# Optimization experiments

Hardware: AMD Instinct MI355X
Metric: run time of the kernel (lower is better)

## Reference

```python
import jax, jax.numpy as jnp
import numpy as np

EMBED_DIM = 1024
NUM_HEADS = 16
DEPTH = EMBED_DIM // NUM_HEADS
SCALE_FACTOR = 0.5
SEQ = 2048
BATCH = 2


def setup_inputs() -> dict:
    key = jax.random.key(0)
    ks = jax.random.split(key, 6)
    x = jax.random.normal(ks[0], (SEQ, BATCH, EMBED_DIM), dtype=jnp.float32)
    attn_mask = jnp.zeros((SEQ, SEQ), dtype=jnp.float32)
    key_padding_mask = jnp.zeros((BATCH, SEQ), dtype=bool)
    # Linear params (torch convention: y = x @ W.T + b)
    s_in = 1.0 / np.sqrt(EMBED_DIM)
    qkv_w = jax.random.uniform(ks[1], (3 * EMBED_DIM, EMBED_DIM), jnp.float32, -s_in, s_in)
    qkv_b = jax.random.uniform(ks[2], (3 * EMBED_DIM,), jnp.float32, -s_in, s_in)
    out_w = jax.random.uniform(ks[3], (EMBED_DIM, EMBED_DIM), jnp.float32, -s_in, s_in)
    out_b = jax.random.uniform(ks[4], (EMBED_DIM,), jnp.float32, -s_in, s_in)
    return {"x": x, "attn_mask": attn_mask, "key_padding_mask": key_padding_mask,
            "qkv_w": qkv_w, "qkv_b": qkv_b, "out_w": out_w, "out_b": out_b}


def reference(x, attn_mask, key_padding_mask, qkv_w, qkv_b, out_w, out_b):
    # x: [S, B, E] -> [B, S, E]
    xb = jnp.transpose(x, (1, 0, 2))
    B, S, E = xb.shape
    qkv = xb @ qkv_w.T + qkv_b                       # [B, S, 3E]
    q, k, v = jnp.split(qkv, 3, axis=2)
    def split_heads(t):                              # [B, S, E] -> [B, H, S, d]
        return jnp.transpose(t.reshape(B, S, NUM_HEADS, DEPTH), (0, 2, 1, 3))
    q, k, v = split_heads(q), split_heads(k), split_heads(v)
    scores = jnp.einsum('bhqd,bhkd->bhqk', q, k) / (DEPTH ** SCALE_FACTOR)
    scores = jnp.where(key_padding_mask[:, None, None, :], -jnp.inf, scores)
    scores = scores + attn_mask[None, None, :, :]
    attn = jax.nn.softmax(scores, axis=-1)           # [B, H, S, S] (dropout p=0)
    wa = jnp.einsum('bhqk,bhkd->bhqd', attn, v)      # [B, H, S, d]
    wa = jnp.transpose(wa, (0, 2, 1, 3)).reshape(B, S, E)
    out = wa @ out_w.T + out_b                       # [B, S, E]
    out = jnp.transpose(out, (1, 0, 2))              # [S, B, E]
    attn_mean = jnp.mean(attn, axis=1)               # [B, S, S]
    return out, attn_mean
```

## Files before the change

### kernel.cpp

```cpp
#include <hip/hip_runtime.h>
#include <hip/hip_bf16.h>


#define Sq 2048
#define Bb 2
#define Ee 1024
#define Hh 16
#define Dd 64
#define LOG2E 1.4426950408889634f
#define QSCALE 0.18033688011112042f

typedef __attribute__((ext_vector_type(8))) short bhalf8;
typedef __attribute__((ext_vector_type(4))) float f32x4;

__device__ __forceinline__ void gld16(const __hip_bfloat16* g, __hip_bfloat16* l) {
    __builtin_amdgcn_global_load_lds(
        (const __attribute__((address_space(1))) unsigned int*)g,
        (__attribute__((address_space(3))) unsigned int*)l, 16, 0, 0);
}

__device__ __forceinline__ int pkbf(float a, float b) {
    union { __hip_bfloat16 h[2]; int i; } u;
    u.h[0] = __float2bfloat16(a);
    u.h[1] = __float2bfloat16(b);
    return u.i;
}

__device__ __forceinline__ int tile_off(int s) {
    return ((s >> 2) & 1) * 2048 + (s >> 7) * 512 + (s & 3) * 128 + ((s >> 3) & 15) * 8;
}

__device__ __forceinline__ int swz(int t) {
    return (t & ~63) | ((t & 7) << 3) | ((t >> 3) & 7);
}

__device__ __forceinline__ int kperm(int p) {
    return (p & 3) | (((p >> 5) & 1) << 2) | ((p & 12) << 1) | (((p >> 4) & 1) << 5);
}

__global__ __launch_bounds__(256) void prep_k(
    const float* __restrict__ x, const float* __restrict__ am,
    const unsigned int* __restrict__ kpm32,
    const float* __restrict__ qkv_w, const float* __restrict__ out_w,
    __hip_bfloat16* __restrict__ xb, __hip_bfloat16* __restrict__ qwb,
    __hip_bfloat16* __restrict__ owb, unsigned int* __restrict__ flag)
{
    const long i = (long)blockIdx.x*256 + threadIdx.x;
    if (i < 1048576) {
        float4 v = ((const float4*)am)[i];
        bool nz = (v.x != 0.f) | (v.y != 0.f) | (v.z != 0.f) | (v.w != 0.f);
        if (i < 1024) nz |= (kpm32[i] != 0u);
        if (__ballot(nz)) { if ((threadIdx.x & 63) == 0) atomicOr(flag, 1u); }
    } else if (i < 2097152) {
        const long j = i - 1048576;
        const int m = (int)(j >> 8), e4 = (int)(j & 255);
        const int b = m >> 11, s = m & 2047;
        float4 v = ((const float4*)x)[(size_t)(s*Bb + b)*256 + e4];
        union { __hip_bfloat16 h[4]; uint2 u; } o;
        o.h[0]=__float2bfloat16(v.x); o.h[1]=__float2bfloat16(v.y);
        o.h[2]=__float2bfloat16(v.z); o.h[3]=__float2bfloat16(v.w);
        ((uint2*)xb)[(size_t)m*256 + e4] = o.u;
    } else if (i < 2883584) {
        const long j = i - 2097152;
        float4 v = ((const float4*)qkv_w)[j];
        union { __hip_bfloat16 h[4]; uint2 u; } o;
        o.h[0]=__float2bfloat16(v.x); o.h[1]=__float2bfloat16(v.y);
        o.h[2]=__float2bfloat16(v.z); o.h[3]=__float2bfloat16(v.w);
        ((uint2*)qwb)[j] = o.u;
    } else if (i < 3145728) {
        const long j = i - 2883584;
        float4 v = ((const float4*)out_w)[j];
        union { __hip_bfloat16 h[4]; uint2 u; } o;
        o.h[0]=__float2bfloat16(v.x); o.h[1]=__float2bfloat16(v.y);
        o.h[2]=__float2bfloat16(v.z); o.h[3]=__float2bfloat16(v.w);
        ((uint2*)owb)[j] = o.u;
    }
}

__global__ __launch_bounds__(256) void gemm_qkv(
    const __hip_bfloat16* __restrict__ A, const __hip_bfloat16* __restrict__ Bw,
    const float* __restrict__ bias,
    __hip_bfloat16* __restrict__ Qp, __hip_bfloat16* __restrict__ Kp,
    __hip_bfloat16* __restrict__ Vt)
{
    __shared__ __align__(16) __hip_bfloat16 As[128*32];
    __shared__ __align__(16) __hip_bfloat16 Bs[128*32];
    const int t = threadIdx.x;
    const int l = t & 63, lm = l & 15, quad = l >> 4;
    const int w = t >> 6;
    const int mw = (w & 1)*64, nw = (w >> 1)*64;
    const int m0 = blockIdx.y*128, n0 = blockIdx.x*128;

    const int srow = t >> 2;
    const int scol = (t & 3)*8;
    const __hip_bfloat16* ag = A  + (size_t)(m0 + srow)*1024 + scol;
    const __hip_bfloat16* bg = Bw + (size_t)(n0 + srow)*1024 + scol;
    __hip_bfloat16* al = As + t*8;
    __hip_bfloat16* bl = Bs + t*8;

    f32x4 acc[4][4] = {};
    for (int k0 = 0; k0 < 1024; k0 += 32) {
        __syncthreads();
        gld16(ag + k0, al);
        gld16(ag + (size_t)64*1024 + k0, al + 2048);
        gld16(bg + k0, bl);
        gld16(bg + (size_t)64*1024 + k0, bl + 2048);
        __syncthreads();
        bhalf8 af[4], bf[4];
#pragma unroll
        for (int i = 0; i < 4; i++) {
            af[i] = *(const bhalf8*)&As[(mw + i*16 + lm)*32 + quad*8];
            bf[i] = *(const bhalf8*)&Bs[(nw + i*16 + lm)*32 + quad*8];
        }
#pragma unroll
        for (int mf = 0; mf < 4; mf++)
#pragma unroll
            for (int nf = 0; nf < 4; nf++)
                acc[mf][nf] = __builtin_amdgcn_mfma_f32_16x16x32_bf16(af[mf], bf[nf], acc[mf][nf], 0,0,0);
    }
#pragma unroll
    for (int nf = 0; nf < 4; nf++) {
        const int n = n0 + nw + nf*16 + lm;
        const float bz = bias[n];
        const int which = n >> 10, hh = (n >> 6) & 15, dd = n & 63;
#pragma unroll
        for (int mf = 0; mf < 4; mf++)
#pragma unroll
            for (int r = 0; r < 4; r++) {
                const int m = m0 + mw + mf*16 + quad*4 + r;
                const int b2 = m >> 11, s2 = m & 2047;
                const float vf = acc[mf][nf][r] + bz;
                if (which == 0)
                    Qp[((size_t)(b2*Hh + hh)*Sq + s2)*Dd + dd] = __float2bfloat16(vf * QSCALE);
                else if (which == 1)
                    Kp[((size_t)(b2*Hh + hh)*Sq + s2)*Dd + dd] = __float2bfloat16(vf);
                else
                    Vt[((size_t)(b2*Hh + hh)*Dd + dd)*Sq + s2] = __float2bfloat16(vf);
            }
    }
}

__global__ __launch_bounds__(256) void attn_mfma(
    const __hip_bfloat16* __restrict__ Qp, const __hip_bfloat16* __restrict__ Kp,
    const __hip_bfloat16* __restrict__ Vt,
    const float* __restrict__ am, const unsigned char* __restrict__ kpm,
    const unsigned int* __restrict__ flag,
    __hip_bfloat16* __restrict__ wa, float* __restrict__ rlbuf)
{
    __shared__ __align__(16) __hip_bfloat16 Ks[4096];
    __shared__ __align__(16) __hip_bfloat16 Vs[4096];
    const int t = threadIdx.x;
    const int w = t >> 6, l = t & 63, lm = l & 15, quad = l >> 4;
    const int blk = blockIdx.x;
    const int xcd = blk & 7;
    const int qt  = (blk >> 3) & 15;
    const int grp = blk >> 7;
    const int bh  = grp*8 + xcd;
    const int b   = bh >> 4, h = bh & 15;
    const int q0  = qt*128 + w*16;
    const bool masked = (flag[0] != 0u);

    const __hip_bfloat16* qbase = Qp + (size_t)bh*Sq*Dd;
    const __hip_bfloat16* kbase = Kp + (size_t)bh*Sq*Dd;
    const __hip_bfloat16* vbase = Vt + (size_t)bh*Dd*Sq;

    bhalf8 bq[2][2];
#pragma unroll
    for (int su = 0; su < 2; su++) {
        const int q = q0 + su*64 + lm;
        bq[su][0] = *(const bhalf8*)(qbase + (size_t)q*Dd + quad*8);
        bq[su][1] = *(const bhalf8*)(qbase + (size_t)q*Dd + quad*8 + 32);
    }

    f32x4 o[2][4] = {};
    float lsum[2] = {0.f, 0.f};

    const int g0 = swz(t), g1 = g0 + 256;
    const int off0 = tile_off(g0), off1 = tile_off(g1);
    const int krow0 = kperm(g0 >> 3);
    const int krow1 = kperm(g1 >> 3);
    const int kcol  = (g0 & 7)*8;
    const int vrow0 = g0 >> 3, vrow1 = g1 >> 3;

    uint4 kreg0 = *(const uint4*)(kbase + (size_t)krow0*Dd + kcol);
    uint4 kreg1 = *(const uint4*)(kbase + (size_t)krow1*Dd + kcol);
    uint4 vreg0 = *(const uint4*)(vbase + (size_t)vrow0*Sq + kcol);
    uint4 vreg1 = *(const uint4*)(vbase + (size_t)vrow1*Sq + kcol);

    for (int kt = 0; kt < 32; kt++) {
        __syncthreads();
        *(uint4*)&Ks[off0] = kreg0;
        *(uint4*)&Ks[off1] = kreg1;
        *(uint4*)&Vs[off0] = vreg0;
        *(uint4*)&Vs[off1] = vreg1;
        if (kt < 31) {
            const int kn = (kt + 1)*64;
            kreg0 = *(const uint4*)(kbase + (size_t)(kn + krow0)*Dd + kcol);
            kreg1 = *(const uint4*)(kbase + (size_t)(kn + krow1)*Dd + kcol);
            vreg0 = *(const uint4*)(vbase + (size_t)vrow0*Sq + kn + kcol);
            vreg1 = *(const uint4*)(vbase + (size_t)vrow1*Sq + kn + kcol);
        }
        __syncthreads();

        const int k0 = kt*64;
        f32x4 s[2][4] = {};
#pragma unroll
        for (int f = 0; f < 2; f++) {
            bhalf8 ak[4];
#pragma unroll
            for (int j = 0; j < 4; j++)
                ak[j] = *(const bhalf8*)&Ks[f*2048 + j*512 + l*8];
#pragma unroll
            for (int su = 0; su < 2; su++)
#pragma unroll
                for (int j = 0; j < 4; j++)
                    s[su][j] = __builtin_amdgcn_mfma_f32_16x16x32_bf16(ak[j], bq[su][f], s[su][j], 0,0,0);
        }

        int pk[2][4][2];
#pragma unroll
        for (int su = 0; su < 2; su++) {
            const int q = q0 + su*64 + lm;
#pragma unroll
            for (int j = 0; j < 4; j++) {
                float p[4];
#pragma unroll
                for (int r = 0; r < 4; r++) {
                    float sv = s[su][j][r];
                    if (masked) {
                        const int key = k0 + 32*(j & 1) + 8*quad + 4*(j >> 1) + r;
                        const float km = kpm[b*Sq + key] ? -1e30f : 0.0f;
                        sv += (am[(size_t)q*Sq + key] + km) * LOG2E;
                    }
                    p[r] = exp2f(sv);
                }
                lsum[su] += (p[0]+p[1]) + (p[2]+p[3]);
                pk[su][j][0] = pkbf(p[0], p[1]);
                pk[su][j][1] = pkbf(p[2], p[3]);
            }
        }

#pragma unroll
        for (int ks = 0; ks < 2; ks++) {
            bhalf8 av[4];
#pragma unroll
            for (int nd = 0; nd < 4; nd++)
                av[nd] = *(const bhalf8*)&Vs[ks*2048 + nd*512 + l*8];
#pragma unroll
            for (int su = 0; su < 2; su++) {
                union { int i[4]; bhalf8 v; } bp;
                bp.i[0] = pk[su][ks][0];
                bp.i[1] = pk[su][ks][1];
                bp.i[2] = pk[su][ks + 2][0];
                bp.i[3] = pk[su][ks + 2][1];
#pragma unroll
                for (int nd = 0; nd < 4; nd++)
                    o[su][nd] = __builtin_amdgcn_mfma_f32_16x16x32_bf16(av[nd], bp.v, o[su][nd], 0,0,0);
            }
        }
    }

#pragma unroll
    for (int su = 0; su < 2; su++) {
        const int q = q0 + su*64 + lm;
        float ls = lsum[su];
        ls += __shfl_xor(ls, 16, 64);
        ls += __shfl_xor(ls, 32, 64);
        const float rl = 1.0f / ls;
        if (quad == 0) rlbuf[(size_t)bh*Sq + q] = rl * 0.0625f;
#pragma unroll
        for (int nd = 0; nd < 4; nd++) {
            union { __hip_bfloat16 hx[4]; uint2 u; } ou;
#pragma unroll
            for (int r = 0; r < 4; r++) ou.hx[r] = __float2bfloat16(o[su][nd][r] * rl);
            *(uint2*)(wa + ((size_t)b*Sq + q)*Ee + h*Dd + nd*16 + quad*4) = ou.u;
        }
    }
}

__global__ __launch_bounds__(256) void attn_mean_k(
    const __hip_bfloat16* __restrict__ Qp, const __hip_bfloat16* __restrict__ Kp,
    const float* __restrict__ am, const unsigned char* __restrict__ kpm,
    const unsigned int* __restrict__ flag,
    const float* __restrict__ rlbuf, float* __restrict__ attn_mean)
{
    __shared__ __align__(16) __hip_bfloat16 Ks[2][4096];
    const int t = threadIdx.x;
    const int w = t >> 6, l = t & 63, lm = l & 15, quad = l >> 4;
    const int blk = blockIdx.x;
    const int q0idx = (blk & 7) | (((blk >> 8) & 1) << 3);
    const int kc    = ((blk >> 3) & 31) * 64;
    const int b     = (blk >> 9) & 1;
    const int q0    = q0idx * 128;
    const bool masked = (flag[0] != 0u);

    const int g0 = swz(t), g1 = g0 + 256;
    const int off0 = tile_off(g0), off1 = tile_off(g1);
    const int qa = q0 + w*32;

    float macc[2][4][4] = {};
    uint4 kr0, kr1;

    {
        const __hip_bfloat16* kg = Kp + ((size_t)(b*Hh)*Sq + kc)*Dd;
        uint4 a0 = *(const uint4*)(kg + (size_t)g0*8);
        uint4 a1 = *(const uint4*)(kg + (size_t)g1*8);
        *(uint4*)&Ks[0][off0] = a0;
        *(uint4*)&Ks[0][off1] = a1;
        const __hip_bfloat16* kg1 = kg + (size_t)Sq*Dd;
        kr0 = *(const uint4*)(kg1 + (size_t)g0*8);
        kr1 = *(const uint4*)(kg1 + (size_t)g1*8);
    }

    for (int h = 0; h < Hh; h++) {
        __syncthreads();
        if (h < Hh - 1) {
            *(uint4*)&Ks[(h + 1) & 1][off0] = kr0;
            *(uint4*)&Ks[(h + 1) & 1][off1] = kr1;
            if (h < Hh - 2) {
                const __hip_bfloat16* kn = Kp + ((size_t)(b*Hh + h + 2)*Sq + kc)*Dd;
                kr0 = *(const uint4*)(kn + (size_t)g0*8);
                kr1 = *(const uint4*)(kn + (size_t)g1*8);
            }
        }

        const size_t base = (size_t)(b*Hh + h)*Sq;
        const __hip_bfloat16* Kc = Ks[h & 1];
#pragma unroll
        for (int su = 0; su < 2; su++) {
            const int qrow = qa + su*16;
            const __hip_bfloat16* qg = Qp + (base + qrow + lm)*Dd + quad*8;
            f32x4 s[4] = {};
#pragma unroll
            for (int f = 0; f < 2; f++) {
                bhalf8 aq = *(const bhalf8*)(qg + f*32);
#pragma unroll
                for (int j = 0; j < 4; j++) {
                    bhalf8 bk = *(const bhalf8*)&Kc[f*2048 + j*512 + l*8];
                    s[j] = __builtin_amdgcn_mfma_f32_16x16x32_bf16(aq, bk, s[j], 0,0,0);
                }
            }
            const f32x4 rl4 = *(const f32x4*)(rlbuf + base + qrow + quad*4);
#pragma unroll
            for (int j = 0; j < 4; j++)
#pragma unroll
                for (int r = 0; r < 4; r++) {
                    float sv = s[j][r];
                    if (masked) {
                        const int key = kc + j*16 + lm;
                        const float km = kpm[b*Sq + key] ? -1e30f : 0.0f;
                        sv += (am[(size_t)(qrow + quad*4 + r)*Sq + key] + km) * LOG2E;
                    }
                    macc[su][j][r] += exp2f(sv) * rl4[r];
                }
        }
    }

#pragma unroll
    for (int su = 0; su < 2; su++)
#pragma unroll
        for (int j = 0; j < 4; j++)
#pragma unroll
            for (int r = 0; r < 4; r++)
                attn_mean[((size_t)b*Sq + qa + su*16 + quad*4 + r)*Sq + kc + j*16 + lm] =
                    macc[su][j][r];
}

__global__ __launch_bounds__(256) void gemm_out(
    const __hip_bfloat16* __restrict__ A, const __hip_bfloat16* __restrict__ Bw,
    const float* __restrict__ bias, float* __restrict__ outp)
{
    __shared__ __align__(16) __hip_bfloat16 As[128*32];
    __shared__ __align__(16) __hip_bfloat16 Bs[128*32];
    const int t = threadIdx.x;
    const int l = t & 63, lm = l & 15, quad = l >> 4;
    const int w = t >> 6;
    const int mw = (w & 1)*64, nw = (w >> 1)*64;
    const int m0 = blockIdx.y*128, n0 = blockIdx.x*128;

    const int srow = t >> 2;
    const int scol = (t & 3)*8;
    const __hip_bfloat16* ag = A  + (size_t)(m0 + srow)*1024 + scol;
    const __hip_bfloat16* bg = Bw + (size_t)(n0 + srow)*1024 + scol;
    __hip_bfloat16* al = As + t*8;
    __hip_bfloat16* bl = Bs + t*8;

    f32x4 acc[4][4] = {};
    for (int k0 = 0; k0 < 1024; k0 += 32) {
        __syncthreads();
        gld16(ag + k0, al);
        gld16(ag + (size_t)64*1024 + k0, al + 2048);
        gld16(bg + k0, bl);
        gld16(bg + (size_t)64*1024 + k0, bl + 2048);
        __syncthreads();
        bhalf8 af[4], bf[4];
#pragma unroll
        for (int i = 0; i < 4; i++) {
            af[i] = *(const bhalf8*)&As[(mw + i*16 + lm)*32 + quad*8];
            bf[i] = *(const bhalf8*)&Bs[(nw + i*16 + lm)*32 + quad*8];
        }
#pragma unroll
        for (int mf = 0; mf < 4; mf++)
#pragma unroll
            for (int nf = 0; nf < 4; nf++)
                acc[mf][nf] = __builtin_amdgcn_mfma_f32_16x16x32_bf16(af[mf], bf[nf], acc[mf][nf], 0,0,0);
    }
#pragma unroll
    for (int nf = 0; nf < 4; nf++) {
        const int n = n0 + nw + nf*16 + lm;
        const float bz = bias[n];
#pragma unroll
        for (int mf = 0; mf < 4; mf++)
#pragma unroll
            for (int r = 0; r < 4; r++) {
                const int m = m0 + mw + mf*16 + quad*4 + r;
                const int b2 = m >> 11, s2 = m & 2047;
                outp[((size_t)s2*Bb + b2)*Ee + n] = acc[mf][nf][r] + bz;
            }
    }
}

extern "C" void kernel_launch(void* const* d_in, const int* in_sizes, int n_in,
                              void* d_out, int out_size, void* d_ws, size_t ws_size,
                              hipStream_t stream) {
    const float*         x         = (const float*)d_in[0];
    const float*         attn_mask = (const float*)d_in[1];
    const unsigned char* kpm       = (const unsigned char*)d_in[2];
    const float*         qkv_w     = (const float*)d_in[3];
    const float*         qkv_b     = (const float*)d_in[4];
    const float*         out_w     = (const float*)d_in[5];
    const float*         out_b     = (const float*)d_in[6];

    float* outp      = (float*)d_out;
    float* attn_mean = outp + 4194304;

    __hip_bfloat16* xb  = (__hip_bfloat16*)d_ws;
    __hip_bfloat16* qwb = xb  + 4194304;
    __hip_bfloat16* owb = qwb + 3145728;
    __hip_bfloat16* Qp  = owb + 1048576;
    __hip_bfloat16* Kp  = Qp  + 4194304;
    __hip_bfloat16* Vt  = Kp  + 4194304;
    __hip_bfloat16* wab = Vt  + 4194304;
    float* rlbuf        = (float*)(wab + 4194304);
    unsigned int* flag  = (unsigned int*)(rlbuf + 65536);

    hipMemsetAsync(flag, 0, sizeof(unsigned int), stream);
    prep_k<<<12288, 256, 0, stream>>>(x, attn_mask, (const unsigned int*)kpm,
                                      qkv_w, out_w, xb, qwb, owb, flag);
    gemm_qkv<<<dim3(24, 32), 256, 0, stream>>>(xb, qwb, qkv_b, Qp, Kp, Vt);
    attn_mfma<<<dim3(512), 256, 0, stream>>>(Qp, Kp, Vt, attn_mask, kpm, flag, wab, rlbuf);
    attn_mean_k<<<dim3(1024), 256, 0, stream>>>(Qp, Kp, attn_mask, kpm, flag, rlbuf, attn_mean);
    gemm_out<<<dim3(8, 32), 256, 0, stream>>>(wab, owb, out_b, outp);
}
```

Measured before the change: 314.4 us.

## Load K/V MFMA operands directly from global, drop LDS staging and barriers

The attention kernel stops staging K and V tiles through shared memory with double-buffered registers and two barriers per iteration. Each wave now loads its MFMA operands straight from global memory (relying on L2/L1 reuse across waves) and raises wave priority around the MFMA blocks. Float-to-bf16 packing is switched to the hardware packed-convert instruction everywhere. The trade is more global/L1 traffic and exposed load latency with no explicit prefetch, in exchange for no LDS writes or block-wide syncs.

```diff
diff --git a/kernel.cpp b/kernel.cpp
--- a/kernel.cpp
+++ b/kernel.cpp
@@ -20,10 +20,9 @@
 }
 
 __device__ __forceinline__ int pkbf(float a, float b) {
-    union { __hip_bfloat16 h[2]; int i; } u;
-    u.h[0] = __float2bfloat16(a);
-    u.h[1] = __float2bfloat16(b);
-    return u.i;
+    int r;
+    asm("v_cvt_pk_bf16_f32 %0, %1, %2" : "=v"(r) : "v"(a), "v"(b));
+    return r;
 }
 
 __device__ __forceinline__ int tile_off(int s) {
@@ -32,10 +31,6 @@
 
 __device__ __forceinline__ int swz(int t) {
     return (t & ~63) | ((t & 7) << 3) | ((t >> 3) & 7);
-}
-
-__device__ __forceinline__ int kperm(int p) {
-    return (p & 3) | (((p >> 5) & 1) << 2) | ((p & 12) << 1) | (((p >> 4) & 1) << 5);
 }
 
 __global__ __launch_bounds__(256) void prep_k(
@@ -56,24 +51,24 @@
         const int m = (int)(j >> 8), e4 = (int)(j & 255);
         const int b = m >> 11, s = m & 2047;
         float4 v = ((const float4*)x)[(size_t)(s*Bb + b)*256 + e4];
-        union { __hip_bfloat16 h[4]; uint2 u; } o;
-        o.h[0]=__float2bfloat16(v.x); o.h[1]=__float2bfloat16(v.y);
-        o.h[2]=__float2bfloat16(v.z); o.h[3]=__float2bfloat16(v.w);
-        ((uint2*)xb)[(size_t)m*256 + e4] = o.u;
+        uint2 o;
+        o.x = (unsigned)pkbf(v.x, v.y);
+        o.y = (unsigned)pkbf(v.z, v.w);
+        ((uint2*)xb)[(size_t)m*256 + e4] = o;
     } else if (i < 2883584) {
         const long j = i - 2097152;
         float4 v = ((const float4*)qkv_w)[j];
-        union { __hip_bfloat16 h[4]; uint2 u; } o;
-        o.h[0]=__float2bfloat16(v.x); o.h[1]=__float2bfloat16(v.y);
-        o.h[2]=__float2bfloat16(v.z); o.h[3]=__float2bfloat16(v.w);
-        ((uint2*)qwb)[j] = o.u;
+        uint2 o;
+        o.x = (unsigned)pkbf(v.x, v.y);
+        o.y = (unsigned)pkbf(v.z, v.w);
+        ((uint2*)qwb)[j] = o;
     } else if (i < 3145728) {
         const long j = i - 2883584;
         float4 v = ((const float4*)out_w)[j];
-        union { __hip_bfloat16 h[4]; uint2 u; } o;
-        o.h[0]=__float2bfloat16(v.x); o.h[1]=__float2bfloat16(v.y);
-        o.h[2]=__float2bfloat16(v.z); o.h[3]=__float2bfloat16(v.w);
-        ((uint2*)owb)[j] = o.u;
+        uint2 o;
+        o.x = (unsigned)pkbf(v.x, v.y);
+        o.y = (unsigned)pkbf(v.z, v.w);
+        ((uint2*)owb)[j] = o;
     }
 }
 
@@ -147,8 +142,6 @@
     const unsigned int* __restrict__ flag,
     __hip_bfloat16* __restrict__ wa, float* __restrict__ rlbuf)
 {
-    __shared__ __align__(16) __hip_bfloat16 Ks[4096];
-    __shared__ __align__(16) __hip_bfloat16 Vs[4096];
     const int t = threadIdx.x;
     const int w = t >> 6, l = t & 63, lm = l & 15, quad = l >> 4;
     const int blk = blockIdx.x;
@@ -172,50 +165,40 @@
         bq[su][1] = *(const bhalf8*)(qbase + (size_t)q*Dd + quad*8 + 32);
     }
 
+    int krA[4];
+#pragma unroll
+    for (int j = 0; j < 4; j++)
+        krA[j] = (lm & 3) | ((j >> 1) << 2) | ((lm & 12) << 1) | ((j & 1) << 5);
+    const __hip_bfloat16* pK = kbase + quad*8;
+    const __hip_bfloat16* pV = vbase + (size_t)lm*Sq + quad*8;
+
     f32x4 o[2][4] = {};
     float lsum[2] = {0.f, 0.f};
 
-    const int g0 = swz(t), g1 = g0 + 256;
-    const int off0 = tile_off(g0), off1 = tile_off(g1);
-    const int krow0 = kperm(g0 >> 3);
-    const int krow1 = kperm(g1 >> 3);
-    const int kcol  = (g0 & 7)*8;
-    const int vrow0 = g0 >> 3, vrow1 = g1 >> 3;
-
-    uint4 kreg0 = *(const uint4*)(kbase + (size_t)krow0*Dd + kcol);
-    uint4 kreg1 = *(const uint4*)(kbase + (size_t)krow1*Dd + kcol);
-    uint4 vreg0 = *(const uint4*)(vbase + (size_t)vrow0*Sq + kcol);
-    uint4 vreg1 = *(const uint4*)(vbase + (size_t)vrow1*Sq + kcol);
-
     for (int kt = 0; kt < 32; kt++) {
-        __syncthreads();
-        *(uint4*)&Ks[off0] = kreg0;
-        *(uint4*)&Ks[off1] = kreg1;
-        *(uint4*)&Vs[off0] = vreg0;
-        *(uint4*)&Vs[off1] = vreg1;
-        if (kt < 31) {
-            const int kn = (kt + 1)*64;
-            kreg0 = *(const uint4*)(kbase + (size_t)(kn + krow0)*Dd + kcol);
-            kreg1 = *(const uint4*)(kbase + (size_t)(kn + krow1)*Dd + kcol);
-            vreg0 = *(const uint4*)(vbase + (size_t)vrow0*Sq + kn + kcol);
-            vreg1 = *(const uint4*)(vbase + (size_t)vrow1*Sq + kn + kcol);
-        }
-        __syncthreads();
-
         const int k0 = kt*64;
+        bhalf8 ak[2][4], av[2][4];
+#pragma unroll
+        for (int f = 0; f < 2; f++)
+#pragma unroll
+            for (int j = 0; j < 4; j++)
+                ak[f][j] = *(const bhalf8*)(pK + (size_t)(k0 + krA[j])*Dd + f*32);
+#pragma unroll
+        for (int ks = 0; ks < 2; ks++)
+#pragma unroll
+            for (int nd = 0; nd < 4; nd++)
+                av[ks][nd] = *(const bhalf8*)(pV + (size_t)(nd*16)*Sq + k0 + ks*32);
+
         f32x4 s[2][4] = {};
-#pragma unroll
-        for (int f = 0; f < 2; f++) {
-            bhalf8 ak[4];
-#pragma unroll
-            for (int j = 0; j < 4; j++)
-                ak[j] = *(const bhalf8*)&Ks[f*2048 + j*512 + l*8];
+        __builtin_amdgcn_s_setprio(1);
+#pragma unroll
+        for (int f = 0; f < 2; f++)
 #pragma unroll
             for (int su = 0; su < 2; su++)
 #pragma unroll
                 for (int j = 0; j < 4; j++)
-                    s[su][j] = __builtin_amdgcn_mfma_f32_16x16x32_bf16(ak[j], bq[su][f], s[su][j], 0,0,0);
-        }
+                    s[su][j] = __builtin_amdgcn_mfma_f32_16x16x32_bf16(ak[f][j], bq[su][f], s[su][j], 0,0,0);
+        __builtin_amdgcn_s_setprio(0);
 
         int pk[2][4][2];
 #pragma unroll
@@ -240,12 +223,9 @@
             }
         }
 
-#pragma unroll
-        for (int ks = 0; ks < 2; ks++) {
-            bhalf8 av[4];
-#pragma unroll
-            for (int nd = 0; nd < 4; nd++)
-                av[nd] = *(const bhalf8*)&Vs[ks*2048 + nd*512 + l*8];
+        __builtin_amdgcn_s_setprio(1);
+#pragma unroll
+        for (int ks = 0; ks < 2; ks++)
 #pragma unroll
             for (int su = 0; su < 2; su++) {
                 union { int i[4]; bhalf8 v; } bp;
@@ -255,9 +235,9 @@
                 bp.i[3] = pk[su][ks + 2][1];
 #pragma unroll
                 for (int nd = 0; nd < 4; nd++)
-                    o[su][nd] = __builtin_amdgcn_mfma_f32_16x16x32_bf16(av[nd], bp.v, o[su][nd], 0,0,0);
-            }
-        }
+                    o[su][nd] = __builtin_amdgcn_mfma_f32_16x16x32_bf16(av[ks][nd], bp.v, o[su][nd], 0,0,0);
+            }
+        __builtin_amdgcn_s_setprio(0);
     }
 
 #pragma unroll
@@ -270,10 +250,10 @@
         if (quad == 0) rlbuf[(size_t)bh*Sq + q] = rl * 0.0625f;
 #pragma unroll
         for (int nd = 0; nd < 4; nd++) {
-            union { __hip_bfloat16 hx[4]; uint2 u; } ou;
-#pragma unroll
-            for (int r = 0; r < 4; r++) ou.hx[r] = __float2bfloat16(o[su][nd][r] * rl);
-            *(uint2*)(wa + ((size_t)b*Sq + q)*Ee + h*Dd + nd*16 + quad*4) = ou.u;
+            uint2 ou;
+            ou.x = (unsigned)pkbf(o[su][nd][0] * rl, o[su][nd][1] * rl);
+            ou.y = (unsigned)pkbf(o[su][nd][2] * rl, o[su][nd][3] * rl);
+            *(uint2*)(wa + ((size_t)b*Sq + q)*Ee + h*Dd + nd*16 + quad*4) = ou;
         }
     }
 }
```

After: 360.5 us. 1.15x slower.
